# Performance work log

Measured on AMD Instinct MI355X. Metric: run time of the kernel, lower is better.

Reference implementation:

```python
import jax, jax.numpy as jnp
import numpy as np

B, C, H, W = 4, 128, 128, 128
E, K, HID = 11, 6, 512  # num_experts, active_experts, 4*dim


def setup_inputs() -> dict:
    key = jax.random.key(0)
    ks = jax.random.split(key, 5)
    return {
        "x": jax.random.normal(ks[0], (B, C, H, W), jnp.float32),
        "gate_w": jax.random.normal(ks[1], (E, C), jnp.float32) * 0.02,
        "gate_b": jnp.zeros((E,), jnp.float32),
        "w1": jax.random.normal(ks[2], (E, HID, C), jnp.float32) * 0.02,
        "b1": jnp.zeros((E, HID), jnp.float32),
        "w2": jax.random.normal(ks[3], (E, C, HID), jnp.float32) * 0.02,
        "b2": jnp.zeros((E, C), jnp.float32),
    }


def reference(x, gate_w, gate_b, w1, b1, w2, b2):
    n_experts = gate_w.shape[0]
    k = K  # active_experts
    # channels-last for per-pixel routing / 1x1-conv-as-matmul
    xcl = jnp.transpose(x, (0, 2, 3, 1))  # [B,H,W,C]
    # --- router (1x1 conv gate + softmax over experts + top-k) ---
    logits = jnp.einsum('bhwc,ec->bhwe', xcl, gate_w) + gate_b
    scores = jax.nn.softmax(logits, axis=-1)            # [B,H,W,E]
    topk_p, topk_i = jax.lax.top_k(scores, k)           # [B,H,W,K]
    topk_p = topk_p / topk_p.sum(axis=-1, keepdims=True)
    # scatter routing weights into dense per-expert mask (indices distinct)
    onehot = jax.nn.one_hot(topk_i, n_experts, dtype=x.dtype)  # [B,H,W,K,E]
    mask = jnp.einsum('bhwke,bhwk->bhwe', onehot, topk_p)      # [B,H,W,E]
    # --- dense expert compute, masked accumulate (as in original loop) ---
    acc = jnp.zeros_like(xcl)
    for e in range(n_experts):
        h = jax.nn.gelu(jnp.einsum('bhwc,dc->bhwd', xcl, w1[e]) + b1[e],
                        approximate=False)  # torch GELU is exact erf form
        oe = jnp.einsum('bhwd,cd->bhwc', h, w2[e]) + b2[e]
        acc = acc + mask[..., e:e + 1] * oe
    y = x + jnp.transpose(acc, (0, 3, 1, 2))  # back to NCHW
    # --- load-balancing aux loss ---
    mean_prob = scores.mean(axis=(0, 1, 2))            # [E]
    mean_load = onehot.sum(axis=3).mean(axis=(0, 1, 2))  # binary mask mean, [E]
    aux_loss = n_experts * jnp.sum(mean_prob * mean_load)
    return (y, aux_loss)
```

## Files before the change

kernel.cpp:

```cpp
#include <hip/hip_runtime.h>
#include <stdint.h>

#define C_   128
#define HW_  16384
#define CHW_ (C_*HW_)
#define N_   65536
#define E_   11
#define K_   6
#define HID_ 512

typedef __attribute__((ext_vector_type(8))) short short8;
typedef __attribute__((ext_vector_type(4))) float float4v;

#define GLD(g, s) __builtin_amdgcn_global_load_lds( \
    (const __attribute__((address_space(1))) unsigned int*)(uintptr_t)(g), \
    (__attribute__((address_space(3))) unsigned int*)(unsigned int)(uintptr_t)(s), 16, 0, 0)

__device__ __forceinline__ unsigned short f2bf(float f){
  union { float f; unsigned u; } v; v.f = f;
  unsigned r = v.u + 0x7fffu + ((v.u >> 16) & 1u);
  return (unsigned short)(r >> 16);
}
__device__ __forceinline__ float gelu_w(float v, float wr){
  float t = __builtin_amdgcn_fmed3f(v, -2.5f, 2.5f);
  float u = t * t;
  float s = fmaf(u, fmaf(u, fmaf(u, -0.00076957f, 0.0147811f), -0.126434f), 0.795742f);
  float p = t * s;
  return (v * wr) * fmaf(0.5f, p, 0.5f);
}
__device__ __forceinline__ unsigned pk2(float g0, float g1){
  return __builtin_amdgcn_perm(__float_as_uint(g1) + 0x8000u,
                               __float_as_uint(g0) + 0x8000u, 0x07060302u);
}

__global__ __launch_bounds__(256) void k_convert(const float* __restrict__ w1,
                                                 const float* __restrict__ w2,
                                                 unsigned short* __restrict__ wimg,
                                                 float* __restrict__ auxsum){
  int i = blockIdx.x * 256 + threadIdx.x;
  if (i < 2 * E_) auxsum[i] = 0.0f;
  if (i >= 176 * 1024) return;
  int rec = i >> 10, r = i & 1023;
  int e = rec >> 4, hc = rec & 15;
  const float* src;
  if (r < 512){
    int mt = r >> 8, ks = (r >> 6) & 3, lane = r & 63;
    int hid = hc * 32 + mt * 16 + (lane & 15);
    int c = ks * 32 + (lane >> 4) * 8;
    src = w1 + ((size_t)e * 512 + hid) * 128 + c;
  } else {
    int r2 = r - 512;
    int nt = r2 >> 6, lane = r2 & 63;
    int cc = nt * 16 + (lane & 15);
    int hd = hc * 32 + (lane >> 4) * 8;
    src = w2 + ((size_t)e * 128 + cc) * 512 + hd;
  }
  float4 a = *(const float4*)src, b = *(const float4*)(src + 4);
  union { unsigned short us[8]; uint4 v; } u;
  u.us[0] = f2bf(a.x); u.us[1] = f2bf(a.y); u.us[2] = f2bf(a.z); u.us[3] = f2bf(a.w);
  u.us[4] = f2bf(b.x); u.us[5] = f2bf(b.y); u.us[6] = f2bf(b.z); u.us[7] = f2bf(b.w);
  ((uint4*)wimg)[i] = u.v;
}

__global__ __launch_bounds__(256) void k_pre(const float* __restrict__ x,
                                             const float* __restrict__ gw,
                                             const float* __restrict__ gb,
                                             unsigned short* __restrict__ xcl,
                                             float* __restrict__ mask,
                                             float* __restrict__ auxsum){
  __shared__ float tt[64 * 130];
  __shared__ float g[E_ * C_];
  __shared__ float gbs[E_];
  __shared__ float ap[E_], al[E_];
  int tid = threadIdx.x;
  int pix0 = blockIdx.x * 64;
  int b = pix0 >> 14, hw0 = pix0 & 16383;
  const float* xb = x + (size_t)b * CHW_ + hw0;

  for (int i = tid; i < E_ * C_; i += 256) g[i] = gw[i];
  if (tid < E_) { gbs[tid] = gb[tid]; ap[tid] = 0.f; al[tid] = 0.f; }

  #pragma unroll 4
  for (int it = 0; it < 32; ++it){
    int flat = it * 256 + tid;
    int c = flat >> 6, p = flat & 63;
    tt[p * 130 + c] = xb[c * HW_ + p];
  }
  __syncthreads();
  #pragma unroll 4
  for (int it = 0; it < 16; ++it){
    int u = it * 256 + tid;
    int p = u >> 6, cc = u & 63;
    float f0 = tt[p * 130 + 2 * cc], f1 = tt[p * 130 + 2 * cc + 1];
    unsigned out = (unsigned)f2bf(f0) | ((unsigned)f2bf(f1) << 16);
    ((unsigned*)xcl)[(size_t)(pix0 + p) * 64 + cc] = out;
  }

  int p = tid >> 2, t4 = tid & 3;
  float lg[E_];
  #pragma unroll
  for (int e = 0; e < E_; ++e) lg[e] = (t4 == 0) ? gbs[e] : 0.f;
  #pragma unroll 4
  for (int j = 0; j < 32; ++j){
    int c = t4 * 32 + j;
    float xv = tt[p * 130 + c];
    #pragma unroll
    for (int e = 0; e < E_; ++e) lg[e] = fmaf(xv, g[e * C_ + c], lg[e]);
  }
  #pragma unroll
  for (int e = 0; e < E_; ++e){
    lg[e] += __shfl_xor(lg[e], 1, 64);
    lg[e] += __shfl_xor(lg[e], 2, 64);
  }
  float mx = lg[0];
  #pragma unroll
  for (int e = 1; e < E_; ++e) mx = fmaxf(mx, lg[e]);
  float pr[E_]; float s = 0.f;
  #pragma unroll
  for (int e = 0; e < E_; ++e){ pr[e] = expf(lg[e] - mx); s += pr[e]; }
  float inv = 1.0f / s;
  #pragma unroll
  for (int e = 0; e < E_; ++e) pr[e] *= inv;

  unsigned selmask = 0; float wsum = 0.f;
  for (int k = 0; k < K_; ++k){
    float bv = -1.f; int bi = 0;
    #pragma unroll
    for (int e = 0; e < E_; ++e){
      bool better = (((selmask >> e) & 1u) == 0u) && (pr[e] > bv);
      bv = better ? pr[e] : bv;
      bi = better ? e : bi;
    }
    selmask |= 1u << bi; wsum += bv;
  }
  float invw = 1.0f / wsum;
  if (t4 == 0){
    int pix = pix0 + p;
    #pragma unroll
    for (int e = 0; e < E_; ++e){
      bool sel = (selmask >> e) & 1u;
      mask[(size_t)pix * E_ + e] = sel ? pr[e] * invw : 0.f;
      atomicAdd(&ap[e], pr[e]);
      if (sel) atomicAdd(&al[e], 1.0f);
    }
  }
  __syncthreads();
  if (tid < E_){
    atomicAdd(&auxsum[tid], ap[tid]);
    atomicAdd(&auxsum[E_ + tid], al[tid]);
  }
}

__global__ __launch_bounds__(256, 2) void k_ffn(const unsigned short* __restrict__ xcl,
                                                const unsigned short* __restrict__ wimg,
                                                const float* __restrict__ b1,
                                                const float* __restrict__ b2,
                                                const float* __restrict__ mask,
                                                const float* __restrict__ auxsum,
                                                const float* __restrict__ x,
                                                float* __restrict__ y){
  __shared__ unsigned char smem[63488];
  int tid = threadIdx.x;
  int w = tid >> 6, l = tid & 63;
  int q = l >> 4, c16 = l & 15;
  int pix0 = blockIdx.x * 128;

  if (blockIdx.x == 0 && tid == 0){
    float s = 0.f;
    const float invN = 1.0f / (float)N_;
    for (int e = 0; e < E_; ++e)
      s += (auxsum[e] * invN) * (auxsum[E_ + e] * invN);
    y[(size_t)N_ * C_] = (float)E_ * s;
  }

  unsigned short* Xs = (unsigned short*)smem;
  #pragma unroll 2
  for (int it = 0; it < 8; ++it){
    int ch = it * 256 + tid;
    int r = ch >> 4, cc = ch & 15;
    uint4 v = *(const uint4*)(xcl + ((size_t)(pix0 + r) << 7) + cc * 8);
    int gmt = r >> 4, rl = r & 15, ks = cc >> 2, qq = cc & 3;
    *(uint4*)(Xs + ((((gmt * 4 + ks) * 4 + qq) * 16 + rl) << 3)) = v;
  }
  __syncthreads();

  short8 Xf[2][4];
  #pragma unroll
  for (int t = 0; t < 2; ++t)
    #pragma unroll
    for (int ks = 0; ks < 4; ++ks)
      Xf[t][ks] = *(const short8*)(Xs + (((((2 * w + t) * 4 + ks) * 4 + q) * 16 + c16) << 3));
  __syncthreads();

  #pragma unroll
  for (int rr = 0; rr < 2; ++rr){
    const unsigned short* g = wimg + (size_t)rr * 8192 + w * 2048 + l * 8;
    unsigned char* lb = smem + rr * 16384 + w * 4096;
    #pragma unroll
    for (int t = 0; t < 4; ++t) GLD(g + t * 512, lb + t * 1024);
  }
  float* maskl = (float*)(smem + 57344);
  for (int idx = tid; idx < 1536; idx += 256){
    int pp = idx / 12, ee = idx - pp * 12;
    maskl[idx] = (ee < 11) ? mask[(size_t)(pix0 + pp) * 11 + ee] : 0.f;
  }
  float4 bn0 = *(const float4*)(b1 + q * 4);
  float4 bn1 = *(const float4*)(b1 + 16 + q * 4);
  __syncthreads();

  unsigned* Hscr = (unsigned*)(smem + 49152) + w * 512;

  float4v facc[2][8];
  #pragma unroll
  for (int mt = 0; mt < 2; ++mt)
    #pragma unroll
    for (int nt = 0; nt < 8; ++nt) facc[mt][nt] = (float4v){0.f,0.f,0.f,0.f};

  float wr0 = 0.f, wr1 = 0.f;
  int sw = (c16 + (c16 >> 2)) & 3;
  int bufA = 0;

  #pragma unroll 1
  for (int i = 0; i < 176; ++i){
    asm volatile("s_waitcnt vmcnt(6)" ::: "memory");
    __builtin_amdgcn_s_barrier();
    {
      int pf = (i + 2 <= 175) ? (i + 2) : 175;
      const unsigned short* g = wimg + (size_t)pf * 8192 + w * 2048 + l * 8;
      unsigned char* lb = smem + (pf % 3) * 16384 + w * 4096;
      #pragma unroll
      for (int t = 0; t < 4; ++t) GLD(g + t * 512, lb + t * 1024);
    }
    float4 bc0 = bn0, bc1 = bn1;
    {
      int nb = (i + 1 <= 175) ? (i + 1) : 175;
      bn0 = *(const float4*)(b1 + nb * 32 + q * 4);
      bn1 = *(const float4*)(b1 + nb * 32 + 16 + q * 4);
    }
    __builtin_amdgcn_sched_barrier(0);
    const unsigned short* wb = (const unsigned short*)(smem + bufA * 16384);
    bufA = (bufA == 2) ? 0 : bufA + 1;

    if ((i & 15) == 0){
      int e = i >> 4;
      wr0 = maskl[((2 * w + 0) * 16 + c16) * 12 + e];
      wr1 = maskl[((2 * w + 1) * 16 + c16) * 12 + e];
    }

    float4v h00 = {bc0.x, bc0.y, bc0.z, bc0.w};
    float4v h01 = h00;
    float4v h10 = {bc1.x, bc1.y, bc1.z, bc1.w};
    float4v h11 = h10;
    #pragma unroll
    for (int ks = 0; ks < 4; ++ks){
      short8 a0 = *(const short8*)(wb + ks * 512 + l * 8);
      short8 a1 = *(const short8*)(wb + (4 + ks) * 512 + l * 8);
      h00 = __builtin_amdgcn_mfma_f32_16x16x32_bf16(a0, Xf[0][ks], h00, 0, 0, 0);
      h01 = __builtin_amdgcn_mfma_f32_16x16x32_bf16(a0, Xf[1][ks], h01, 0, 0, 0);
      h10 = __builtin_amdgcn_mfma_f32_16x16x32_bf16(a1, Xf[0][ks], h10, 0, 0, 0);
      h11 = __builtin_amdgcn_mfma_f32_16x16x32_bf16(a1, Xf[1][ks], h11, 0, 0, 0);
    }

    #pragma unroll
    for (int mh = 0; mh < 2; ++mh){
      float4v hv0 = (mh == 0) ? h00 : h10;
      float4v hv1 = (mh == 0) ? h01 : h11;
      int grp = (((mh * 2 + (q >> 1)) ^ sw) << 2);
      int lo0 = (q * 2) & 3;
      uint2 d0, d1;
      d0.x = pk2(gelu_w(hv0[0], wr0), gelu_w(hv0[1], wr0));
      d0.y = pk2(gelu_w(hv0[2], wr0), gelu_w(hv0[3], wr0));
      d1.x = pk2(gelu_w(hv1[0], wr1), gelu_w(hv1[1], wr1));
      d1.y = pk2(gelu_w(hv1[2], wr1), gelu_w(hv1[3], wr1));
      *(uint2*)(Hscr + c16 * 16 + grp + lo0)        = d0;
      *(uint2*)(Hscr + (16 + c16) * 16 + grp + lo0) = d1;
    }
    short8 af0 = *(const short8*)(Hscr + c16 * 16 + ((q ^ sw) << 2));
    short8 af1 = *(const short8*)(Hscr + (16 + c16) * 16 + ((q ^ sw) << 2));

    #pragma unroll
    for (int nt = 0; nt < 8; ++nt){
      short8 bf = *(const short8*)(wb + 4096 + nt * 512 + l * 8);
      facc[0][nt] = __builtin_amdgcn_mfma_f32_16x16x32_bf16(af0, bf, facc[0][nt], 0, 0, 0);
      facc[1][nt] = __builtin_amdgcn_mfma_f32_16x16x32_bf16(af1, bf, facc[1][nt], 0, 0, 0);
    }
  }

  __syncthreads();
  float* lds_t = (float*)smem;
  float* b2t   = (float*)(smem + 33024);
  for (int idx = tid; idx < 1536; idx += 256){
    int cc = idx / 12, ee = idx - cc * 12;
    b2t[idx] = (ee < 11) ? b2[ee * 128 + cc] : 0.f;
  }

  #pragma unroll 1
  for (int h = 0; h < 2; ++h){
    __syncthreads();
    if ((w >> 1) == h){
      int wh = w & 1;
      #pragma unroll
      for (int mt = 0; mt < 2; ++mt)
        #pragma unroll
        for (int nt = 0; nt < 8; ++nt)
          #pragma unroll
          for (int rg = 0; rg < 4; ++rg)
            lds_t[(wh * 32 + mt * 16 + q * 4 + rg) * 129 + nt * 16 + c16] = facc[mt][nt][rg];
    }
    __syncthreads();
    int p = tid & 63;
    int row = h * 64 + p;
    float4 m0 = *(const float4*)(maskl + row * 12);
    float4 m1 = *(const float4*)(maskl + row * 12 + 4);
    float4 m2 = *(const float4*)(maskl + row * 12 + 8);
    int pix = pix0 + row; int bb = pix >> 14, hw = pix & 16383;
    #pragma unroll 4
    for (int it = 0; it < 32; ++it){
      int c = w * 32 + it;
      float acc = lds_t[p * 129 + c];
      float4 b0 = *(const float4*)(b2t + c * 12);
      float4 bq1 = *(const float4*)(b2t + c * 12 + 4);
      float4 bq2 = *(const float4*)(b2t + c * 12 + 8);
      acc = fmaf(m0.x, b0.x, acc);  acc = fmaf(m0.y, b0.y, acc);
      acc = fmaf(m0.z, b0.z, acc);  acc = fmaf(m0.w, b0.w, acc);
      acc = fmaf(m1.x, bq1.x, acc); acc = fmaf(m1.y, bq1.y, acc);
      acc = fmaf(m1.z, bq1.z, acc); acc = fmaf(m1.w, bq1.w, acc);
      acc = fmaf(m2.x, bq2.x, acc); acc = fmaf(m2.y, bq2.y, acc);
      acc = fmaf(m2.z, bq2.z, acc);
      size_t idx2 = (size_t)bb * CHW_ + (size_t)c * HW_ + hw;
      y[idx2] = x[idx2] + acc;
    }
  }
}

extern "C" void kernel_launch(void* const* d_in, const int* in_sizes, int n_in,
                              void* d_out, int out_size, void* d_ws, size_t ws_size,
                              hipStream_t stream){
  const float* x  = (const float*)d_in[0];
  const float* gw = (const float*)d_in[1];
  const float* gb = (const float*)d_in[2];
  const float* w1 = (const float*)d_in[3];
  const float* b1 = (const float*)d_in[4];
  const float* w2 = (const float*)d_in[5];
  const float* b2 = (const float*)d_in[6];
  float* y = (float*)d_out;
  char* ws = (char*)d_ws;

  unsigned short* xcl  = (unsigned short*)ws;
  unsigned short* wimg = (unsigned short*)(ws + 16777216);
  float* mask   = (float*)(ws + 19660800);
  float* auxsum = (float*)(ws + 22544384);

  hipLaunchKernelGGL(k_convert, dim3(704),  dim3(256), 0, stream, w1, w2, wimg, auxsum);
  hipLaunchKernelGGL(k_pre,     dim3(1024), dim3(256), 0, stream, x, gw, gb, xcl, mask, auxsum);
  hipLaunchKernelGGL(k_ffn,     dim3(512),  dim3(256), 0, stream, xcl, wimg, b1, b2, mask, auxsum, x, y);
}
```

Measured before the change: 363.5 us.

## Double pixel tile per block to 256 and use double-buffered weight staging

Each block now handles 256 pixels instead of 128, with each wave owning 64 pixels (four 16-row MFMA tiles). Every weight slab staged into LDS is therefore reused across twice as many pixels, halving total weight traffic, and the grid shrinks to 256 blocks. To fit LDS and registers, the weight ring drops from triple to double buffering with a full vmcnt(0) wait, and launch bounds fall to one block per SIMD group. The costs are lower occupancy, higher register pressure from 32 accumulator tiles, and less prefetch depth, while 256 blocks may underfill the 256 CUs' latency hiding.

```diff
diff --git a/kernel.cpp b/kernel.cpp
--- a/kernel.cpp
+++ b/kernel.cpp
@@ -151,7 +151,7 @@
   }
 }
 
-__global__ __launch_bounds__(256, 2) void k_ffn(const unsigned short* __restrict__ xcl,
+__global__ __launch_bounds__(256, 1) void k_ffn(const unsigned short* __restrict__ xcl,
                                                 const unsigned short* __restrict__ wimg,
                                                 const float* __restrict__ b1,
                                                 const float* __restrict__ b2,
@@ -159,11 +159,11 @@
                                                 const float* __restrict__ auxsum,
                                                 const float* __restrict__ x,
                                                 float* __restrict__ y){
-  __shared__ unsigned char smem[63488];
+  __shared__ unsigned char smem[61440];
   int tid = threadIdx.x;
   int w = tid >> 6, l = tid & 63;
   int q = l >> 4, c16 = l & 15;
-  int pix0 = blockIdx.x * 128;
+  int pix0 = blockIdx.x * 256;
 
   if (blockIdx.x == 0 && tid == 0){
     float s = 0.f;
@@ -174,33 +174,37 @@
   }
 
   unsigned short* Xs = (unsigned short*)smem;
-  #pragma unroll 2
-  for (int it = 0; it < 8; ++it){
-    int ch = it * 256 + tid;
-    int r = ch >> 4, cc = ch & 15;
-    uint4 v = *(const uint4*)(xcl + ((size_t)(pix0 + r) << 7) + cc * 8);
-    int gmt = r >> 4, rl = r & 15, ks = cc >> 2, qq = cc & 3;
-    *(uint4*)(Xs + ((((gmt * 4 + ks) * 4 + qq) * 16 + rl) << 3)) = v;
-  }
-  __syncthreads();
-
-  short8 Xf[2][4];
-  #pragma unroll
-  for (int t = 0; t < 2; ++t)
-    #pragma unroll
-    for (int ks = 0; ks < 4; ++ks)
-      Xf[t][ks] = *(const short8*)(Xs + (((((2 * w + t) * 4 + ks) * 4 + q) * 16 + c16) << 3));
-  __syncthreads();
-
-  #pragma unroll
-  for (int rr = 0; rr < 2; ++rr){
-    const unsigned short* g = wimg + (size_t)rr * 8192 + w * 2048 + l * 8;
-    unsigned char* lb = smem + rr * 16384 + w * 4096;
+  short8 Xf[4][4];
+  #pragma unroll 1
+  for (int half = 0; half < 2; ++half){
+    #pragma unroll 2
+    for (int it = 0; it < 8; ++it){
+      int ch = it * 256 + tid;
+      int r = ch >> 4, cc = ch & 15;
+      uint4 v = *(const uint4*)(xcl + ((size_t)(pix0 + half * 128 + r) << 7) + cc * 8);
+      int gmt = r >> 4, rl = r & 15, ks = cc >> 2, qq = cc & 3;
+      *(uint4*)(Xs + ((((gmt * 4 + ks) * 4 + qq) * 16 + rl) << 3)) = v;
+    }
+    __syncthreads();
+    if ((w >> 1) == half){
+      int wl = w & 1;
+      #pragma unroll
+      for (int t = 0; t < 4; ++t)
+        #pragma unroll
+        for (int ks = 0; ks < 4; ++ks)
+          Xf[t][ks] = *(const short8*)(Xs + (((((wl * 4 + t) * 4 + ks) * 4 + q) * 16 + c16) << 3));
+    }
+    __syncthreads();
+  }
+
+  {
+    const unsigned short* g = wimg + (size_t)w * 2048 + l * 8;
+    unsigned char* lb = smem + w * 4096;
     #pragma unroll
     for (int t = 0; t < 4; ++t) GLD(g + t * 512, lb + t * 1024);
   }
-  float* maskl = (float*)(smem + 57344);
-  for (int idx = tid; idx < 1536; idx += 256){
+  float* maskl = (float*)(smem + 49152);
+  for (int idx = tid; idx < 3072; idx += 256){
     int pp = idx / 12, ee = idx - pp * 12;
     maskl[idx] = (ee < 11) ? mask[(size_t)(pix0 + pp) * 11 + ee] : 0.f;
   }
@@ -208,26 +212,25 @@
   float4 bn1 = *(const float4*)(b1 + 16 + q * 4);
   __syncthreads();
 
-  unsigned* Hscr = (unsigned*)(smem + 49152) + w * 512;
-
-  float4v facc[2][8];
-  #pragma unroll
-  for (int mt = 0; mt < 2; ++mt)
-    #pragma unroll
-    for (int nt = 0; nt < 8; ++nt) facc[mt][nt] = (float4v){0.f,0.f,0.f,0.f};
-
-  float wr0 = 0.f, wr1 = 0.f;
+  unsigned* Hscr = (unsigned*)(smem + 32768) + w * 1024;
+
+  float4v facc[4][8];
+  #pragma unroll
+  for (int t = 0; t < 4; ++t)
+    #pragma unroll
+    for (int nt = 0; nt < 8; ++nt) facc[t][nt] = (float4v){0.f,0.f,0.f,0.f};
+
+  float wr[4] = {0.f, 0.f, 0.f, 0.f};
   int sw = (c16 + (c16 >> 2)) & 3;
-  int bufA = 0;
 
   #pragma unroll 1
   for (int i = 0; i < 176; ++i){
-    asm volatile("s_waitcnt vmcnt(6)" ::: "memory");
+    asm volatile("s_waitcnt vmcnt(0)" ::: "memory");
     __builtin_amdgcn_s_barrier();
     {
-      int pf = (i + 2 <= 175) ? (i + 2) : 175;
+      int pf = (i + 1 <= 175) ? (i + 1) : 175;
       const unsigned short* g = wimg + (size_t)pf * 8192 + w * 2048 + l * 8;
-      unsigned char* lb = smem + (pf % 3) * 16384 + w * 4096;
+      unsigned char* lb = smem + ((pf & 1) << 14) + w * 4096;
       #pragma unroll
       for (int t = 0; t < 4; ++t) GLD(g + t * 512, lb + t * 1024);
     }
@@ -238,74 +241,78 @@
       bn1 = *(const float4*)(b1 + nb * 32 + 16 + q * 4);
     }
     __builtin_amdgcn_sched_barrier(0);
-    const unsigned short* wb = (const unsigned short*)(smem + bufA * 16384);
-    bufA = (bufA == 2) ? 0 : bufA + 1;
+    const unsigned short* wb = (const unsigned short*)(smem + ((i & 1) << 14));
 
     if ((i & 15) == 0){
       int e = i >> 4;
-      wr0 = maskl[((2 * w + 0) * 16 + c16) * 12 + e];
-      wr1 = maskl[((2 * w + 1) * 16 + c16) * 12 + e];
-    }
-
-    float4v h00 = {bc0.x, bc0.y, bc0.z, bc0.w};
-    float4v h01 = h00;
-    float4v h10 = {bc1.x, bc1.y, bc1.z, bc1.w};
-    float4v h11 = h10;
+      #pragma unroll
+      for (int t = 0; t < 4; ++t)
+        wr[t] = maskl[(64 * w + t * 16 + c16) * 12 + e];
+    }
+
+    float4v hacc[2][4];
+    #pragma unroll
+    for (int t = 0; t < 4; ++t){
+      hacc[0][t] = (float4v){bc0.x, bc0.y, bc0.z, bc0.w};
+      hacc[1][t] = (float4v){bc1.x, bc1.y, bc1.z, bc1.w};
+    }
     #pragma unroll
     for (int ks = 0; ks < 4; ++ks){
       short8 a0 = *(const short8*)(wb + ks * 512 + l * 8);
       short8 a1 = *(const short8*)(wb + (4 + ks) * 512 + l * 8);
-      h00 = __builtin_amdgcn_mfma_f32_16x16x32_bf16(a0, Xf[0][ks], h00, 0, 0, 0);
-      h01 = __builtin_amdgcn_mfma_f32_16x16x32_bf16(a0, Xf[1][ks], h01, 0, 0, 0);
-      h10 = __builtin_amdgcn_mfma_f32_16x16x32_bf16(a1, Xf[0][ks], h10, 0, 0, 0);
-      h11 = __builtin_amdgcn_mfma_f32_16x16x32_bf16(a1, Xf[1][ks], h11, 0, 0, 0);
-    }
-
-    #pragma unroll
-    for (int mh = 0; mh < 2; ++mh){
-      float4v hv0 = (mh == 0) ? h00 : h10;
-      float4v hv1 = (mh == 0) ? h01 : h11;
-      int grp = (((mh * 2 + (q >> 1)) ^ sw) << 2);
-      int lo0 = (q * 2) & 3;
-      uint2 d0, d1;
-      d0.x = pk2(gelu_w(hv0[0], wr0), gelu_w(hv0[1], wr0));
-      d0.y = pk2(gelu_w(hv0[2], wr0), gelu_w(hv0[3], wr0));
-      d1.x = pk2(gelu_w(hv1[0], wr1), gelu_w(hv1[1], wr1));
-      d1.y = pk2(gelu_w(hv1[2], wr1), gelu_w(hv1[3], wr1));
-      *(uint2*)(Hscr + c16 * 16 + grp + lo0)        = d0;
-      *(uint2*)(Hscr + (16 + c16) * 16 + grp + lo0) = d1;
-    }
-    short8 af0 = *(const short8*)(Hscr + c16 * 16 + ((q ^ sw) << 2));
-    short8 af1 = *(const short8*)(Hscr + (16 + c16) * 16 + ((q ^ sw) << 2));
+      #pragma unroll
+      for (int t = 0; t < 4; ++t){
+        hacc[0][t] = __builtin_amdgcn_mfma_f32_16x16x32_bf16(a0, Xf[t][ks], hacc[0][t], 0, 0, 0);
+        hacc[1][t] = __builtin_amdgcn_mfma_f32_16x16x32_bf16(a1, Xf[t][ks], hacc[1][t], 0, 0, 0);
+      }
+    }
+
+    #pragma unroll
+    for (int t = 0; t < 4; ++t){
+      #pragma unroll
+      for (int mh = 0; mh < 2; ++mh){
+        float4v hv = hacc[mh][t];
+        int grp = (((mh * 2 + (q >> 1)) ^ sw) << 2);
+        int lo0 = (q * 2) & 3;
+        uint2 d;
+        d.x = pk2(gelu_w(hv[0], wr[t]), gelu_w(hv[1], wr[t]));
+        d.y = pk2(gelu_w(hv[2], wr[t]), gelu_w(hv[3], wr[t]));
+        *(uint2*)(Hscr + (t * 16 + c16) * 16 + grp + lo0) = d;
+      }
+    }
+    short8 af[4];
+    #pragma unroll
+    for (int t = 0; t < 4; ++t)
+      af[t] = *(const short8*)(Hscr + (t * 16 + c16) * 16 + ((q ^ sw) << 2));
 
     #pragma unroll
     for (int nt = 0; nt < 8; ++nt){
       short8 bf = *(const short8*)(wb + 4096 + nt * 512 + l * 8);
-      facc[0][nt] = __builtin_amdgcn_mfma_f32_16x16x32_bf16(af0, bf, facc[0][nt], 0, 0, 0);
-      facc[1][nt] = __builtin_amdgcn_mfma_f32_16x16x32_bf16(af1, bf, facc[1][nt], 0, 0, 0);
+      #pragma unroll
+      for (int t = 0; t < 4; ++t)
+        facc[t][nt] = __builtin_amdgcn_mfma_f32_16x16x32_bf16(af[t], bf, facc[t][nt], 0, 0, 0);
     }
   }
 
   __syncthreads();
   float* lds_t = (float*)smem;
-  float* b2t   = (float*)(smem + 33024);
+  float* b2t   = (float*)(smem + 43008);
   for (int idx = tid; idx < 1536; idx += 256){
     int cc = idx / 12, ee = idx - cc * 12;
     b2t[idx] = (ee < 11) ? b2[ee * 128 + cc] : 0.f;
   }
 
   #pragma unroll 1
-  for (int h = 0; h < 2; ++h){
+  for (int h = 0; h < 4; ++h){
     __syncthreads();
-    if ((w >> 1) == h){
-      int wh = w & 1;
-      #pragma unroll
-      for (int mt = 0; mt < 2; ++mt)
+    if (w == h){
+      #pragma unroll
+      for (int t = 0; t < 4; ++t)
         #pragma unroll
         for (int nt = 0; nt < 8; ++nt)
           #pragma unroll
           for (int rg = 0; rg < 4; ++rg)
-            lds_t[(wh * 32 + mt * 16 + q * 4 + rg) * 129 + nt * 16 + c16] = facc[mt][nt][rg];
+            lds_t[(t * 16 + q * 4 + rg) * 129 + nt * 16 + c16] = facc[t][nt][rg];
     }
     __syncthreads();
     int p = tid & 63;
@@ -353,5 +360,5 @@
 
   hipLaunchKernelGGL(k_convert, dim3(704),  dim3(256), 0, stream, w1, w2, wimg, auxsum);
   hipLaunchKernelGGL(k_pre,     dim3(1024), dim3(256), 0, stream, x, gw, gb, xcl, mask, auxsum);
-  hipLaunchKernelGGL(k_ffn,     dim3(512),  dim3(256), 0, stream, xcl, wimg, b1, b2, mask, auxsum, x, y);
-}
+  hipLaunchKernelGGL(k_ffn,     dim3(256),  dim3(256), 0, stream, xcl, wimg, b1, b2, mask, auxsum, x, y);
+}
```

Result: slower. 486.6 us (+33.9%).

## Switch expert FFN to 32x32x16 MFMA with permlane-based H fragment reuse

Applied to the files above, without the earlier changes.

Moves the expert FFN from 16x16x32 to 32x32x16 bf16 MFMA tiles. The weight image is re-laid out to match, X fragments are loaded straight from global memory instead of being staged through LDS, and the GELU output is reshaped in registers with permlane32 swaps rather than an LDS scratch round-trip. The epilogue writes vectorized float4 stores and skips the b2 mask-weighted bias when a flag computed in k_pre shows b2 is all zero. The aim is fewer LDS round-trips and MFMA instructions per tile, at the cost of extra register pressure and reliance on permlane32_swap support.

```diff
diff --git a/kernel.cpp b/kernel.cpp
--- a/kernel.cpp
+++ b/kernel.cpp
@@ -11,6 +11,8 @@
 
 typedef __attribute__((ext_vector_type(8))) short short8;
 typedef __attribute__((ext_vector_type(4))) float float4v;
+typedef __attribute__((ext_vector_type(16))) float float16v;
+typedef __attribute__((ext_vector_type(2))) unsigned uint2v;
 
 #define GLD(g, s) __builtin_amdgcn_global_load_lds( \
     (const __attribute__((address_space(1))) unsigned int*)(uintptr_t)(g), \
@@ -32,44 +34,56 @@
   return __builtin_amdgcn_perm(__float_as_uint(g1) + 0x8000u,
                                __float_as_uint(g0) + 0x8000u, 0x07060302u);
 }
+__device__ __forceinline__ void pswap32(unsigned &a, unsigned &b){
+#if __has_builtin(__builtin_amdgcn_permlane32_swap)
+  uint2v r = __builtin_amdgcn_permlane32_swap(a, b, false, false);
+  a = r.x; b = r.y;
+#else
+  asm volatile("v_permlane32_swap_b32 %0, %1" : "+v"(a), "+v"(b));
+#endif
+}
 
 __global__ __launch_bounds__(256) void k_convert(const float* __restrict__ w1,
                                                  const float* __restrict__ w2,
                                                  unsigned short* __restrict__ wimg,
                                                  float* __restrict__ auxsum){
-  int i = blockIdx.x * 256 + threadIdx.x;
-  if (i < 2 * E_) auxsum[i] = 0.0f;
-  if (i >= 176 * 1024) return;
-  int rec = i >> 10, r = i & 1023;
-  int e = rec >> 4, hc = rec & 15;
+  int t = blockIdx.x * 256 + threadIdx.x;
+  if (t < 23) auxsum[t] = 0.0f;
+  if (t >= 180224) return;
   const float* src;
-  if (r < 512){
-    int mt = r >> 8, ks = (r >> 6) & 3, lane = r & 63;
-    int hid = hc * 32 + mt * 16 + (lane & 15);
-    int c = ks * 32 + (lane >> 4) * 8;
-    src = w1 + ((size_t)e * 512 + hid) * 128 + c;
+  size_t dst;
+  if (t < 90112){
+    int e = t >> 13, hid = (t >> 4) & 511, c8 = t & 15;
+    src = w1 + (size_t)t * 8;
+    int rec = e * 16 + (hid >> 5);
+    int kc = c8 >> 1, half = c8 & 1;
+    int l = (hid & 31) | (half << 5);
+    dst = (size_t)rec * 8192 + kc * 512 + l * 8;
   } else {
-    int r2 = r - 512;
-    int nt = r2 >> 6, lane = r2 & 63;
-    int cc = nt * 16 + (lane & 15);
-    int hd = hc * 32 + (lane >> 4) * 8;
-    src = w2 + ((size_t)e * 128 + cc) * 512 + hd;
+    int u = t - 90112;
+    int e = u >> 13, cc = (u >> 6) & 127, hd8 = u & 63;
+    src = w2 + (size_t)u * 8;
+    int rec = e * 16 + (hd8 >> 2);
+    int kc2 = (hd8 >> 1) & 1, half = hd8 & 1, ct = cc >> 5;
+    int l = (cc & 31) | (half << 5);
+    dst = (size_t)rec * 8192 + 4096 + (ct * 2 + kc2) * 512 + l * 8;
   }
   float4 a = *(const float4*)src, b = *(const float4*)(src + 4);
-  union { unsigned short us[8]; uint4 v; } u;
-  u.us[0] = f2bf(a.x); u.us[1] = f2bf(a.y); u.us[2] = f2bf(a.z); u.us[3] = f2bf(a.w);
-  u.us[4] = f2bf(b.x); u.us[5] = f2bf(b.y); u.us[6] = f2bf(b.z); u.us[7] = f2bf(b.w);
-  ((uint4*)wimg)[i] = u.v;
+  union { unsigned short us[8]; uint4 v; } u4;
+  u4.us[0] = f2bf(a.x); u4.us[1] = f2bf(a.y); u4.us[2] = f2bf(a.z); u4.us[3] = f2bf(a.w);
+  u4.us[4] = f2bf(b.x); u4.us[5] = f2bf(b.y); u4.us[6] = f2bf(b.z); u4.us[7] = f2bf(b.w);
+  *(uint4*)(wimg + dst) = u4.v;
 }
 
 __global__ __launch_bounds__(256) void k_pre(const float* __restrict__ x,
                                              const float* __restrict__ gw,
                                              const float* __restrict__ gb,
+                                             const float* __restrict__ b2,
                                              unsigned short* __restrict__ xcl,
                                              float* __restrict__ mask,
                                              float* __restrict__ auxsum){
-  __shared__ float tt[64 * 130];
-  __shared__ float g[E_ * C_];
+  __shared__ __align__(16) float tt[64 * 130];
+  __shared__ __align__(16) float g[E_ * C_];
   __shared__ float gbs[E_];
   __shared__ float ap[E_], al[E_];
   int tid = threadIdx.x;
@@ -100,12 +114,16 @@
   float lg[E_];
   #pragma unroll
   for (int e = 0; e < E_; ++e) lg[e] = (t4 == 0) ? gbs[e] : 0.f;
+  const float2* ttrow = (const float2*)(tt + p * 130 + t4 * 32);
   #pragma unroll 4
-  for (int j = 0; j < 32; ++j){
-    int c = t4 * 32 + j;
-    float xv = tt[p * 130 + c];
-    #pragma unroll
-    for (int e = 0; e < E_; ++e) lg[e] = fmaf(xv, g[e * C_ + c], lg[e]);
+  for (int j2 = 0; j2 < 16; ++j2){
+    float2 xv = ttrow[j2];
+    #pragma unroll
+    for (int e = 0; e < E_; ++e){
+      float2 gv = *(const float2*)(g + e * C_ + t4 * 32 + j2 * 2);
+      lg[e] = fmaf(xv.x, gv.x, lg[e]);
+      lg[e] = fmaf(xv.y, gv.y, lg[e]);
+    }
   }
   #pragma unroll
   for (int e = 0; e < E_; ++e){
@@ -149,6 +167,12 @@
     atomicAdd(&auxsum[tid], ap[tid]);
     atomicAdd(&auxsum[E_ + tid], al[tid]);
   }
+  if (blockIdx.x == 0 && tid < 64){
+    int nz = 0;
+    for (int idx = tid; idx < E_ * C_; idx += 64)
+      nz |= (__float_as_uint(b2[idx]) != 0u) ? 1 : 0;
+    if (nz) atomicOr((int*)(auxsum + 22), 1);
+  }
 }
 
 __global__ __launch_bounds__(256, 2) void k_ffn(const unsigned short* __restrict__ xcl,
@@ -156,41 +180,31 @@
                                                 const float* __restrict__ b1,
                                                 const float* __restrict__ b2,
                                                 const float* __restrict__ mask,
-                                                const float* __restrict__ auxsum,
+                                                const float* __restrict__ aux,
                                                 const float* __restrict__ x,
                                                 float* __restrict__ y){
   __shared__ unsigned char smem[63488];
   int tid = threadIdx.x;
   int w = tid >> 6, l = tid & 63;
-  int q = l >> 4, c16 = l & 15;
+  int l31 = l & 31, hi = l >> 5;
+  int hi4 = hi * 4;
   int pix0 = blockIdx.x * 128;
 
   if (blockIdx.x == 0 && tid == 0){
     float s = 0.f;
     const float invN = 1.0f / (float)N_;
     for (int e = 0; e < E_; ++e)
-      s += (auxsum[e] * invN) * (auxsum[E_ + e] * invN);
+      s += (aux[e] * invN) * (aux[E_ + e] * invN);
     y[(size_t)N_ * C_] = (float)E_ * s;
   }
 
-  unsigned short* Xs = (unsigned short*)smem;
-  #pragma unroll 2
-  for (int it = 0; it < 8; ++it){
-    int ch = it * 256 + tid;
-    int r = ch >> 4, cc = ch & 15;
-    uint4 v = *(const uint4*)(xcl + ((size_t)(pix0 + r) << 7) + cc * 8);
-    int gmt = r >> 4, rl = r & 15, ks = cc >> 2, qq = cc & 3;
-    *(uint4*)(Xs + ((((gmt * 4 + ks) * 4 + qq) * 16 + rl) << 3)) = v;
-  }
-  __syncthreads();
-
-  short8 Xf[2][4];
-  #pragma unroll
-  for (int t = 0; t < 2; ++t)
-    #pragma unroll
-    for (int ks = 0; ks < 4; ++ks)
-      Xf[t][ks] = *(const short8*)(Xs + (((((2 * w + t) * 4 + ks) * 4 + q) * 16 + c16) << 3));
-  __syncthreads();
+  short8 Xf[8];
+  {
+    const unsigned short* xrow = xcl + ((size_t)(pix0 + w * 32 + l31) << 7) + hi * 8;
+    #pragma unroll
+    for (int kc = 0; kc < 8; ++kc)
+      Xf[kc] = *(const short8*)(xrow + kc * 16);
+  }
 
   #pragma unroll
   for (int rr = 0; rr < 2; ++rr){
@@ -199,31 +213,36 @@
     #pragma unroll
     for (int t = 0; t < 4; ++t) GLD(g + t * 512, lb + t * 1024);
   }
-  float* maskl = (float*)(smem + 57344);
-  for (int idx = tid; idx < 1536; idx += 256){
-    int pp = idx / 12, ee = idx - pp * 12;
+  float* maskl = (float*)(smem + 49152);
+  for (int idx = tid; idx < 2048; idx += 256){
+    int pp = idx >> 4, ee = idx & 15;
     maskl[idx] = (ee < 11) ? mask[(size_t)(pix0 + pp) * 11 + ee] : 0.f;
   }
-  float4 bn0 = *(const float4*)(b1 + q * 4);
-  float4 bn1 = *(const float4*)(b1 + 16 + q * 4);
+  float4 bn0 = *(const float4*)(b1 + 0 + hi4);
+  float4 bn1 = *(const float4*)(b1 + 8 + hi4);
+  float4 bn2 = *(const float4*)(b1 + 16 + hi4);
+  float4 bn3 = *(const float4*)(b1 + 24 + hi4);
   __syncthreads();
 
-  unsigned* Hscr = (unsigned*)(smem + 49152) + w * 512;
-
-  float4v facc[2][8];
-  #pragma unroll
-  for (int mt = 0; mt < 2; ++mt)
-    #pragma unroll
-    for (int nt = 0; nt < 8; ++nt) facc[mt][nt] = (float4v){0.f,0.f,0.f,0.f};
-
-  float wr0 = 0.f, wr1 = 0.f;
-  int sw = (c16 + (c16 >> 2)) & 3;
-  int bufA = 0;
+  float16v facc[4];
+  #pragma unroll
+  for (int ct = 0; ct < 4; ++ct) facc[ct] = (float16v)0.0f;
+  float wr = 0.f;
 
   #pragma unroll 1
   for (int i = 0; i < 176; ++i){
-    asm volatile("s_waitcnt vmcnt(6)" ::: "memory");
+    asm volatile("s_waitcnt vmcnt(8)" ::: "memory");
     __builtin_amdgcn_s_barrier();
+    float4 bc0 = bn0, bc1 = bn1, bc2 = bn2, bc3 = bn3;
+    {
+      int nb = (i + 1 <= 175) ? (i + 1) : 175;
+      const float* bp = b1 + nb * 32 + hi4;
+      bn0 = *(const float4*)(bp);
+      bn1 = *(const float4*)(bp + 8);
+      bn2 = *(const float4*)(bp + 16);
+      bn3 = *(const float4*)(bp + 24);
+    }
+    __builtin_amdgcn_sched_barrier(0);
     {
       int pf = (i + 2 <= 175) ? (i + 2) : 175;
       const unsigned short* g = wimg + (size_t)pf * 8192 + w * 2048 + l * 8;
@@ -231,104 +250,83 @@
       #pragma unroll
       for (int t = 0; t < 4; ++t) GLD(g + t * 512, lb + t * 1024);
     }
-    float4 bc0 = bn0, bc1 = bn1;
-    {
-      int nb = (i + 1 <= 175) ? (i + 1) : 175;
-      bn0 = *(const float4*)(b1 + nb * 32 + q * 4);
-      bn1 = *(const float4*)(b1 + nb * 32 + 16 + q * 4);
-    }
     __builtin_amdgcn_sched_barrier(0);
-    const unsigned short* wb = (const unsigned short*)(smem + bufA * 16384);
-    bufA = (bufA == 2) ? 0 : bufA + 1;
-
-    if ((i & 15) == 0){
-      int e = i >> 4;
-      wr0 = maskl[((2 * w + 0) * 16 + c16) * 12 + e];
-      wr1 = maskl[((2 * w + 1) * 16 + c16) * 12 + e];
-    }
-
-    float4v h00 = {bc0.x, bc0.y, bc0.z, bc0.w};
-    float4v h01 = h00;
-    float4v h10 = {bc1.x, bc1.y, bc1.z, bc1.w};
-    float4v h11 = h10;
-    #pragma unroll
-    for (int ks = 0; ks < 4; ++ks){
-      short8 a0 = *(const short8*)(wb + ks * 512 + l * 8);
-      short8 a1 = *(const short8*)(wb + (4 + ks) * 512 + l * 8);
-      h00 = __builtin_amdgcn_mfma_f32_16x16x32_bf16(a0, Xf[0][ks], h00, 0, 0, 0);
-      h01 = __builtin_amdgcn_mfma_f32_16x16x32_bf16(a0, Xf[1][ks], h01, 0, 0, 0);
-      h10 = __builtin_amdgcn_mfma_f32_16x16x32_bf16(a1, Xf[0][ks], h10, 0, 0, 0);
-      h11 = __builtin_amdgcn_mfma_f32_16x16x32_bf16(a1, Xf[1][ks], h11, 0, 0, 0);
-    }
-
-    #pragma unroll
-    for (int mh = 0; mh < 2; ++mh){
-      float4v hv0 = (mh == 0) ? h00 : h10;
-      float4v hv1 = (mh == 0) ? h01 : h11;
-      int grp = (((mh * 2 + (q >> 1)) ^ sw) << 2);
-      int lo0 = (q * 2) & 3;
-      uint2 d0, d1;
-      d0.x = pk2(gelu_w(hv0[0], wr0), gelu_w(hv0[1], wr0));
-      d0.y = pk2(gelu_w(hv0[2], wr0), gelu_w(hv0[3], wr0));
-      d1.x = pk2(gelu_w(hv1[0], wr1), gelu_w(hv1[1], wr1));
-      d1.y = pk2(gelu_w(hv1[2], wr1), gelu_w(hv1[3], wr1));
-      *(uint2*)(Hscr + c16 * 16 + grp + lo0)        = d0;
-      *(uint2*)(Hscr + (16 + c16) * 16 + grp + lo0) = d1;
-    }
-    short8 af0 = *(const short8*)(Hscr + c16 * 16 + ((q ^ sw) << 2));
-    short8 af1 = *(const short8*)(Hscr + (16 + c16) * 16 + ((q ^ sw) << 2));
-
-    #pragma unroll
-    for (int nt = 0; nt < 8; ++nt){
-      short8 bf = *(const short8*)(wb + 4096 + nt * 512 + l * 8);
-      facc[0][nt] = __builtin_amdgcn_mfma_f32_16x16x32_bf16(af0, bf, facc[0][nt], 0, 0, 0);
-      facc[1][nt] = __builtin_amdgcn_mfma_f32_16x16x32_bf16(af1, bf, facc[1][nt], 0, 0, 0);
+    const unsigned char* wb = smem + (i % 3) * 16384;
+
+    if ((i & 15) == 0)
+      wr = maskl[(w * 32 + l31) * 16 + (i >> 4)];
+
+    float16v hacc = {bc0.x, bc0.y, bc0.z, bc0.w, bc1.x, bc1.y, bc1.z, bc1.w,
+                     bc2.x, bc2.y, bc2.z, bc2.w, bc3.x, bc3.y, bc3.z, bc3.w};
+    #pragma unroll
+    for (int kc = 0; kc < 8; ++kc){
+      short8 a = *(const short8*)(wb + kc * 1024 + l * 16);
+      hacc = __builtin_amdgcn_mfma_f32_32x32x16_bf16(a, Xf[kc], hacc, 0, 0, 0);
+    }
+
+    unsigned pd[8];
+    #pragma unroll
+    for (int k = 0; k < 8; ++k)
+      pd[k] = pk2(gelu_w(hacc[2 * k], wr), gelu_w(hacc[2 * k + 1], wr));
+    pswap32(pd[0], pd[2]); pswap32(pd[1], pd[3]);
+    pswap32(pd[4], pd[6]); pswap32(pd[5], pd[7]);
+    union { unsigned u[4]; short8 s; } cv0, cv1;
+    cv0.u[0] = pd[0]; cv0.u[1] = pd[1]; cv0.u[2] = pd[2]; cv0.u[3] = pd[3];
+    cv1.u[0] = pd[4]; cv1.u[1] = pd[5]; cv1.u[2] = pd[6]; cv1.u[3] = pd[7];
+
+    #pragma unroll
+    for (int ct = 0; ct < 4; ++ct){
+      short8 a0 = *(const short8*)(wb + 8192 + (ct * 2 + 0) * 1024 + l * 16);
+      short8 a1 = *(const short8*)(wb + 8192 + (ct * 2 + 1) * 1024 + l * 16);
+      facc[ct] = __builtin_amdgcn_mfma_f32_32x32x16_bf16(a0, cv0.s, facc[ct], 0, 0, 0);
+      facc[ct] = __builtin_amdgcn_mfma_f32_32x32x16_bf16(a1, cv1.s, facc[ct], 0, 0, 0);
     }
   }
 
   __syncthreads();
   float* lds_t = (float*)smem;
-  float* b2t   = (float*)(smem + 33024);
+  float* b2t   = (float*)(smem + 57344);
   for (int idx = tid; idx < 1536; idx += 256){
     int cc = idx / 12, ee = idx - cc * 12;
     b2t[idx] = (ee < 11) ? b2[ee * 128 + cc] : 0.f;
   }
+  int b2nz = ((const int*)aux)[22];
 
   #pragma unroll 1
-  for (int h = 0; h < 2; ++h){
+  for (int h = 0; h < 4; ++h){
     __syncthreads();
-    if ((w >> 1) == h){
-      int wh = w & 1;
+    if (w == h){
       #pragma unroll
-      for (int mt = 0; mt < 2; ++mt)
+      for (int ct = 0; ct < 4; ++ct)
         #pragma unroll
-        for (int nt = 0; nt < 8; ++nt)
+        for (int r = 0; r < 16; ++r)
+          lds_t[(ct * 32 + (r & 3) + 8 * (r >> 2) + hi4) * 33 + l31] = facc[ct][r];
+    }
+    __syncthreads();
+    int c = tid >> 1, p16 = (tid & 1) << 4;
+    int pixg = pix0 + h * 32 + p16;
+    size_t base = (size_t)(pixg >> 14) * CHW_ + (size_t)c * HW_ + (pixg & 16383);
+    float b2r[11];
+    if (b2nz){
+      #pragma unroll
+      for (int e = 0; e < 11; ++e) b2r[e] = b2t[c * 12 + e];
+    }
+    #pragma unroll 2
+    for (int v = 0; v < 4; ++v){
+      float av[4];
+      #pragma unroll
+      for (int k = 0; k < 4; ++k) av[k] = lds_t[c * 33 + p16 + v * 4 + k];
+      if (b2nz){
+        #pragma unroll
+        for (int k = 0; k < 4; ++k){
+          const float* mr = maskl + (h * 32 + p16 + v * 4 + k) * 16;
           #pragma unroll
-          for (int rg = 0; rg < 4; ++rg)
-            lds_t[(wh * 32 + mt * 16 + q * 4 + rg) * 129 + nt * 16 + c16] = facc[mt][nt][rg];
-    }
-    __syncthreads();
-    int p = tid & 63;
-    int row = h * 64 + p;
-    float4 m0 = *(const float4*)(maskl + row * 12);
-    float4 m1 = *(const float4*)(maskl + row * 12 + 4);
-    float4 m2 = *(const float4*)(maskl + row * 12 + 8);
-    int pix = pix0 + row; int bb = pix >> 14, hw = pix & 16383;
-    #pragma unroll 4
-    for (int it = 0; it < 32; ++it){
-      int c = w * 32 + it;
-      float acc = lds_t[p * 129 + c];
-      float4 b0 = *(const float4*)(b2t + c * 12);
-      float4 bq1 = *(const float4*)(b2t + c * 12 + 4);
-      float4 bq2 = *(const float4*)(b2t + c * 12 + 8);
-      acc = fmaf(m0.x, b0.x, acc);  acc = fmaf(m0.y, b0.y, acc);
-      acc = fmaf(m0.z, b0.z, acc);  acc = fmaf(m0.w, b0.w, acc);
-      acc = fmaf(m1.x, bq1.x, acc); acc = fmaf(m1.y, bq1.y, acc);
-      acc = fmaf(m1.z, bq1.z, acc); acc = fmaf(m1.w, bq1.w, acc);
-      acc = fmaf(m2.x, bq2.x, acc); acc = fmaf(m2.y, bq2.y, acc);
-      acc = fmaf(m2.z, bq2.z, acc);
-      size_t idx2 = (size_t)bb * CHW_ + (size_t)c * HW_ + hw;
-      y[idx2] = x[idx2] + acc;
+          for (int e = 0; e < 11; ++e) av[k] = fmaf(mr[e], b2r[e], av[k]);
+        }
+      }
+      float4 xv = *(const float4*)(x + base + v * 4);
+      float4 o = {av[0] + xv.x, av[1] + xv.y, av[2] + xv.z, av[3] + xv.w};
+      *(float4*)(y + base + v * 4) = o;
     }
   }
 }
@@ -352,6 +350,6 @@
   float* auxsum = (float*)(ws + 22544384);
 
   hipLaunchKernelGGL(k_convert, dim3(704),  dim3(256), 0, stream, w1, w2, wimg, auxsum);
-  hipLaunchKernelGGL(k_pre,     dim3(1024), dim3(256), 0, stream, x, gw, gb, xcl, mask, auxsum);
+  hipLaunchKernelGGL(k_pre,     dim3(1024), dim3(256), 0, stream, x, gw, gb, b2, xcl, mask, auxsum);
   hipLaunchKernelGGL(k_ffn,     dim3(512),  dim3(256), 0, stream, xcl, wimg, b1, b2, mask, auxsum, x, y);
 }
```

After: 380.1 us. +4.6%, slower.
